# Kernel tuning notes

Measured on AMD Instinct MI355X. Metric: run time of the kernel, lower is better.

The kernel has to match this reference:

```python
import jax, jax.numpy as jnp
import numpy as np

D_MODEL = 256

def setup_inputs() -> dict:
    key = jax.random.key(0)
    k_x, k_wqkv, k_bqkv, k_wp, k_bp = jax.random.split(key, 5)
    B, T, d = 4, 4096, D_MODEL
    bound_qkv = 1.0 / np.sqrt(d)
    return {
        "x": jax.random.normal(k_x, (B, T, d), dtype=jnp.float32),
        "W_qkv": jax.random.uniform(k_wqkv, (d, 3 * d), jnp.float32, -bound_qkv, bound_qkv),
        "b_qkv": jax.random.uniform(k_bqkv, (3 * d,), jnp.float32, -bound_qkv, bound_qkv),
        "W_proj": jax.random.uniform(k_wp, (d, d), jnp.float32, -bound_qkv, bound_qkv),
        "b_proj": jax.random.uniform(k_bp, (d,), jnp.float32, -bound_qkv, bound_qkv),
    }

def reference(x, W_qkv, b_qkv, W_proj, b_proj):
    B, T, d = x.shape
    qkv = x @ W_qkv + b_qkv                       # (B, T, 3d)
    q, k, v = jnp.split(qkv, 3, axis=-1)          # each (B, T, d)
    scale = 1.0 / np.sqrt(d).astype(np.float32)
    scores = jnp.einsum('btd,bsd->bts', q, k) * scale   # (B, T, T)
    causal = jnp.tril(jnp.ones((T, T), dtype=bool))     # allowed positions
    scores = jnp.where(causal, scores, -jnp.inf)
    weights = jax.nn.softmax(scores, axis=-1)           # (B, T, T)
    ctx = jnp.einsum('bts,bsd->btd', weights, v)        # (B, T, d)
    return ctx @ W_proj + b_proj
```

## Files before the change

### kernel.cpp

```cpp
#include <hip/hip_runtime.h>
#include <math.h>

#define TT 4096
#define BB 4
#define DM 256
#define NSEG_B 80

typedef __attribute__((ext_vector_type(8))) short short8;
typedef __attribute__((ext_vector_type(4))) short short4v;
typedef __attribute__((ext_vector_type(4))) float f32x4;

#define MFMA16(a, b, c) __builtin_amdgcn_mfma_f32_16x16x32_bf16(a, b, c, 0, 0, 0)

#define GL2LDS(gp, lp) __builtin_amdgcn_global_load_lds( \
    (const __attribute__((address_space(1))) unsigned int*)(gp), \
    (__attribute__((address_space(3))) unsigned int*)(lp), 16, 0, 0)

__device__ __forceinline__ short f2b(float f) {
    union { float f; unsigned u; } v; v.f = f;
    unsigned r = v.u + 0x7FFFu + ((v.u >> 16) & 1u);
    return (short)(r >> 16);
}
__device__ __forceinline__ float b2f(short h) {
    union { unsigned u; float f; } v;
    v.u = ((unsigned)(unsigned short)h) << 16;
    return v.f;
}

__global__ __launch_bounds__(256) void transpose_cast2(
    const float* __restrict__ W1, short* __restrict__ Wt1,
    const float* __restrict__ W2, short* __restrict__ Wt2)
{
    __shared__ float T[64 * 68];
    const int tid = threadIdx.x;
    const int by = blockIdx.y;
    const float* W; short* Wt; int N, n0;
    if (by < 12) { W = W1; Wt = Wt1; N = 768; n0 = by * 64; }
    else         { W = W2; Wt = Wt2; N = 256; n0 = (by - 12) * 64; }
    const int k0 = blockIdx.x * 64;
#pragma unroll
    for (int it = 0; it < 4; ++it) {
        int idx = tid + it * 256;
        int r = idx >> 4, c4 = idx & 15;
        *(float4*)&T[r * 68 + c4 * 4] =
            *(const float4*)&W[(size_t)(k0 + r) * N + n0 + c4 * 4];
    }
    __syncthreads();
#pragma unroll
    for (int it = 0; it < 4; ++it) {
        int idx = tid + it * 256;
        int n = idx >> 4, c4 = idx & 15;
        short4v t;
#pragma unroll
        for (int j = 0; j < 4; ++j) t[j] = f2b(T[(c4 * 4 + j) * 68 + n]);
        *(short4v*)&Wt[(size_t)(n0 + n) * 256 + k0 + c4 * 4] = t;
    }
}

__global__ __launch_bounds__(256) void qkv_gemm(
    const float* __restrict__ x, const short* __restrict__ Bt,
    const float* __restrict__ bias, short* __restrict__ qkvb,
    short* __restrict__ VtG)
{
    __shared__ short As[16384];
    __shared__ short Bs[16384];
    __shared__ short Ts[64 * 72];

    const int tid = threadIdx.x;
    const int w = tid >> 6, lane = tid & 63;
    const int l15 = lane & 15, quad = lane >> 4;
    const int m0 = blockIdx.x * 64;
    const int nsup = blockIdx.y * 384;

#pragma unroll
    for (int it = 0; it < 8; ++it) {
        int idx = tid + it * 256;
        int row = ((idx >> 9) << 4) + (idx & 15);
        int col = ((idx >> 6) & 7) * 32 + ((idx >> 4) & 3) * 8;
        const float* src = &x[(size_t)(m0 + row) * 256 + col];
        float4 u = *(const float4*)src, u2 = *(const float4*)(src + 4);
        short8 t;
        t[0] = f2b(u.x);  t[1] = f2b(u.y);  t[2] = f2b(u.z);  t[3] = f2b(u.w);
        t[4] = f2b(u2.x); t[5] = f2b(u2.y); t[6] = f2b(u2.z); t[7] = f2b(u2.w);
        *(short8*)&As[idx * 8] = t;
    }

    for (int t6 = 0; t6 < 6; ++t6) {
        const int n0 = nsup + t6 * 64;
#pragma unroll
        for (int it = 0; it < 8; ++it) {
            int idx = tid + it * 256;
            int n = ((idx >> 9) << 4) + (idx & 15);
            int col = ((idx >> 6) & 7) * 32 + ((idx >> 4) & 3) * 8;
            *(short8*)&Bs[idx * 8] = *(const short8*)&Bt[(size_t)(n0 + n) * 256 + col];
        }
        __syncthreads();

        f32x4 acc[4];
#pragma unroll
        for (int t = 0; t < 4; ++t) acc[t] = (f32x4){0.f, 0.f, 0.f, 0.f};
#pragma unroll
        for (int k0 = 0; k0 < 8; ++k0) {
            short8 a = *(const short8*)&As[((w * 8 + k0) * 64 + lane) * 8];
#pragma unroll
            for (int nt = 0; nt < 4; ++nt) {
                short8 bb = *(const short8*)&Bs[((nt * 8 + k0) * 64 + lane) * 8];
                acc[nt] = MFMA16(a, bb, acc[nt]);
            }
        }

        if (n0 < 512) {
#pragma unroll
            for (int nt = 0; nt < 4; ++nt) {
                int n = n0 + nt * 16 + l15;
                float bv = bias[n];
#pragma unroll
                for (int r = 0; r < 4; ++r)
                    qkvb[(size_t)(m0 + w * 16 + quad * 4 + r) * 768 + n]
                        = f2b(acc[nt][r] + bv);
            }
            __syncthreads();
        } else {
#pragma unroll
            for (int nt = 0; nt < 4; ++nt) {
                int n = n0 + nt * 16 + l15;
                float bv = bias[n];
#pragma unroll
                for (int r = 0; r < 4; ++r)
                    Ts[(nt * 16 + l15) * 72 + w * 16 + quad * 4 + r]
                        = f2b(acc[nt][r] + bv);
            }
            __syncthreads();
            const int d  = tid >> 2;
            const int c  = tid & 3;
            short8 v0 = *(const short8*)&Ts[d * 72 + c * 16];
            short8 v1 = *(const short8*)&Ts[d * 72 + c * 16 + 8];
            const int bg = m0 >> 12, key0 = (m0 & 4095) + c * 16;
            short* dst = &VtG[((size_t)bg * 256 + (n0 - 512) + d) * 4096 + key0];
            *(short8*)dst = v0;
            *(short8*)(dst + 8) = v1;
        }
    }
}

__global__ __launch_bounds__(256, 2) void flash_mfma(
    const short* __restrict__ qkv,
    const short* __restrict__ VtG,
    short* __restrict__ Opart,
    float* __restrict__ L)
{
    __shared__ short Ks[2][4096];
    __shared__ short Vs[8192];
    __shared__ short Ps[4096];

    const int tid = threadIdx.x;
    const int w = tid >> 6, lane = tid & 63;
    const int l15 = lane & 15, quad = lane >> 4;

    const int b = blockIdx.x & 3;
    const int e = (NSEG_B - 1) - (blockIdx.x >> 2);
    const int lid = b * NSEG_B + e;
    int g = 0;
    while (g < 3 && e >= 4 * (g + 1) * (g + 2)) ++g;
    int off = e - 4 * g * (g + 1);
    int qt = 8 * g + off / (g + 1);
    int s  = off - (off / (g + 1)) * (g + 1);
    const int kp_lo = s * 32;
    const int kp_hi = min(kp_lo + 32, 4 * (qt + 1));
    const int npairs = kp_hi - kp_lo;

    const size_t base = (size_t)b * TT * 768;
    const int row0 = qt * 128;

    short8 aq[2][8];
#pragma unroll
    for (int rs = 0; rs < 2; ++rs) {
        const short* qrow = &qkv[base + (size_t)(row0 + rs * 64 + w * 16 + l15) * 768 + quad * 8];
#pragma unroll
        for (int k0 = 0; k0 < 8; ++k0)
            aq[rs][k0] = *(const short8*)&qrow[k0 * 32];
    }

#pragma unroll
    for (int it = 0; it < 2; ++it) {
        int idx = tid + it * 256;
        int row = idx & 15;
        int col = ((idx >> 6) & 7) * 32 + ((idx >> 4) & 3) * 8;
        GL2LDS(&qkv[base + (size_t)(kp_lo * 32 + row) * 768 + 256 + col], &Ks[0][idx * 8]);
    }

    f32x4 o[2][16];
#pragma unroll
    for (int rs = 0; rs < 2; ++rs)
#pragma unroll
        for (int c = 0; c < 16; ++c) o[rs][c] = (f32x4){0.f, 0.f, 0.f, 0.f};
    float l_acc[2][4] = {{0.f, 0.f, 0.f, 0.f}, {0.f, 0.f, 0.f, 0.f}};

    for (int u = 0; u < npairs; ++u) {
        const int j0 = (kp_lo + u) * 32;

        __syncthreads();

#pragma unroll
        for (int it = 0; it < 2; ++it) {
            int idx = tid + it * 256;
            int row = idx & 15;
            int col = ((idx >> 6) & 7) * 32 + ((idx >> 4) & 3) * 8;
            GL2LDS(&qkv[base + (size_t)(j0 + 16 + row) * 768 + 256 + col], &Ks[1][idx * 8]);
        }
        __builtin_amdgcn_sched_barrier(0);
#pragma unroll
        for (int it = 0; it < 4; ++it) {
            int idx = tid + it * 256;
            int d  = ((idx >> 6) << 4) + (idx & 15);
            int kc = ((idx >> 4) & 3) * 8;
            GL2LDS(&VtG[((size_t)b * 256 + d) * 4096 + j0 + kc], &Vs[idx * 8]);
        }
        __builtin_amdgcn_sched_barrier(0);

        {
            f32x4 s4[2];
            s4[0] = (f32x4){0.f, 0.f, 0.f, 0.f};
            s4[1] = (f32x4){0.f, 0.f, 0.f, 0.f};
#pragma unroll
            for (int k0 = 0; k0 < 8; ++k0) {
                short8 bb = *(const short8*)&Ks[0][(k0 * 64 + lane) * 8];
                s4[0] = MFMA16(aq[0][k0], bb, s4[0]);
                s4[1] = MFMA16(aq[1][k0], bb, s4[1]);
            }
#pragma unroll
            for (int rs = 0; rs < 2; ++rs)
#pragma unroll
                for (int r = 0; r < 4; ++r) {
                    const int rg = row0 + rs * 64 + w * 16 + quad * 4 + r;
                    int jg = j0 + l15;
                    float xx = s4[rs][r] * 0.0625f;
                    if (jg > rg) xx = -INFINITY;
                    float pv = __expf(fminf(xx, 30.f));
                    l_acc[rs][r] += pv;
                    Ps[((rs * 4 + w) * 64 + (0 * 2 + (l15 >> 3)) * 16 + quad * 4 + r) * 8
                       + (l15 & 7)] = f2b(pv);
                }
        }

        asm volatile("s_waitcnt vmcnt(4)" ::: "memory");
        __builtin_amdgcn_s_barrier();
        __builtin_amdgcn_sched_barrier(0);

        if (u + 1 < npairs) {
#pragma unroll
            for (int it = 0; it < 2; ++it) {
                int idx = tid + it * 256;
                int row = idx & 15;
                int col = ((idx >> 6) & 7) * 32 + ((idx >> 4) & 3) * 8;
                GL2LDS(&qkv[base + (size_t)(j0 + 32 + row) * 768 + 256 + col], &Ks[0][idx * 8]);
            }
        }
        __builtin_amdgcn_sched_barrier(0);

        {
            f32x4 s4[2];
            s4[0] = (f32x4){0.f, 0.f, 0.f, 0.f};
            s4[1] = (f32x4){0.f, 0.f, 0.f, 0.f};
#pragma unroll
            for (int k0 = 0; k0 < 8; ++k0) {
                short8 bb = *(const short8*)&Ks[1][(k0 * 64 + lane) * 8];
                s4[0] = MFMA16(aq[0][k0], bb, s4[0]);
                s4[1] = MFMA16(aq[1][k0], bb, s4[1]);
            }
#pragma unroll
            for (int rs = 0; rs < 2; ++rs)
#pragma unroll
                for (int r = 0; r < 4; ++r) {
                    const int rg = row0 + rs * 64 + w * 16 + quad * 4 + r;
                    int jg = j0 + 16 + l15;
                    float xx = s4[rs][r] * 0.0625f;
                    if (jg > rg) xx = -INFINITY;
                    float pv = __expf(fminf(xx, 30.f));
                    l_acc[rs][r] += pv;
                    Ps[((rs * 4 + w) * 64 + (1 * 2 + (l15 >> 3)) * 16 + quad * 4 + r) * 8
                       + (l15 & 7)] = f2b(pv);
                }
        }

        if (u + 1 < npairs) {
            asm volatile("s_waitcnt vmcnt(2)" ::: "memory");
        } else {
            asm volatile("s_waitcnt vmcnt(0)" ::: "memory");
        }
        __builtin_amdgcn_s_barrier();
        __builtin_amdgcn_sched_barrier(0);

        {
            short8 a0 = *(const short8*)&Ps[((0 * 4 + w) * 64 + lane) * 8];
            short8 a1 = *(const short8*)&Ps[((1 * 4 + w) * 64 + lane) * 8];
#pragma unroll
            for (int ct = 0; ct < 16; ++ct) {
                short8 bb = *(const short8*)&Vs[(ct * 64 + lane) * 8];
                o[0][ct] = MFMA16(a0, bb, o[0][ct]);
                o[1][ct] = MFMA16(a1, bb, o[1][ct]);
            }
        }
    }

#pragma unroll
    for (int rs = 0; rs < 2; ++rs)
#pragma unroll
        for (int r = 0; r < 4; ++r) {
            float l = l_acc[rs][r];
            l += __shfl_xor(l, 1); l += __shfl_xor(l, 2);
            l += __shfl_xor(l, 4); l += __shfl_xor(l, 8);
            if (l15 == 0)
                L[(size_t)lid * 128 + rs * 64 + w * 16 + quad * 4 + r] = l;
        }
    const size_t ob = (size_t)lid * (128 * 256);
#pragma unroll
    for (int rs = 0; rs < 2; ++rs)
#pragma unroll
        for (int r = 0; r < 4; ++r) {
            int lr = rs * 64 + w * 16 + quad * 4 + r;
#pragma unroll
            for (int c = 0; c < 16; ++c)
                Opart[ob + (size_t)lr * 256 + c * 16 + l15] = f2b(o[rs][c][r]);
        }
}

__global__ __launch_bounds__(256) void proj_gemm(
    const short* __restrict__ Opart, const float* __restrict__ L,
    const short* __restrict__ Bt, const float* __restrict__ bias,
    float* __restrict__ out)
{
    __shared__ short As[8192];
    __shared__ short Bs[16384];
    __shared__ float Linv[32];

    const int tid = threadIdx.x;
    const int w = tid >> 6, lane = tid & 63;
    const int l15 = lane & 15, quad = lane >> 4;
    const int t = blockIdx.x;
    const int b = t >> 7, q32 = t & 127;
    const int qt = q32 >> 2;
    const int ro = (q32 & 3) * 32;
    const int gg = qt >> 3, rr = qt & 7;
    const int sbase = b * NSEG_B + 4 * gg * (gg + 1) + rr * (gg + 1);
    const int nseg = gg + 1;
    const int m0 = t * 32;

    if (tid < 32) {
        float l = 0.f;
#pragma unroll
        for (int s2 = 0; s2 < 4; ++s2)
            if (s2 < nseg) l += L[(size_t)(sbase + s2) * 128 + ro + tid];
        Linv[tid] = 1.f / l;
    }
    __syncthreads();

#pragma unroll
    for (int it = 0; it < 4; ++it) {
        int idx = tid + it * 256;
        int row = ((idx >> 9) << 4) + (idx & 15);
        int col = ((idx >> 6) & 7) * 32 + ((idx >> 4) & 3) * 8;
        float a8[8] = {0.f, 0.f, 0.f, 0.f, 0.f, 0.f, 0.f, 0.f};
#pragma unroll
        for (int s2 = 0; s2 < 4; ++s2) {
            if (s2 < nseg) {
                short8 hv = *(const short8*)&Opart[(size_t)(sbase + s2) * 32768
                                                   + (size_t)(ro + row) * 256 + col];
#pragma unroll
                for (int j = 0; j < 8; ++j) a8[j] += b2f(hv[j]);
            }
        }
        float inv = Linv[row];
        short8 t8;
#pragma unroll
        for (int j = 0; j < 8; ++j) t8[j] = f2b(a8[j] * inv);
        *(short8*)&As[idx * 8] = t8;
    }

    for (int t2 = 0; t2 < 4; ++t2) {
        const int n0 = t2 * 64;
#pragma unroll
        for (int it = 0; it < 8; ++it) {
            int idx = tid + it * 256;
            int n = ((idx >> 9) << 4) + (idx & 15);
            int col = ((idx >> 6) & 7) * 32 + ((idx >> 4) & 3) * 8;
            *(short8*)&Bs[idx * 8] = *(const short8*)&Bt[(size_t)(n0 + n) * 256 + col];
        }
        __syncthreads();

        f32x4 acc[2];
        acc[0] = (f32x4){0.f, 0.f, 0.f, 0.f};
        acc[1] = (f32x4){0.f, 0.f, 0.f, 0.f};
#pragma unroll
        for (int k0 = 0; k0 < 8; ++k0) {
            short8 a = *(const short8*)&As[(((w & 1) * 8 + k0) * 64 + lane) * 8];
#pragma unroll
            for (int nt = 0; nt < 2; ++nt) {
                int n16 = (w >> 1) * 2 + nt;
                short8 bb = *(const short8*)&Bs[((n16 * 8 + k0) * 64 + lane) * 8];
                acc[nt] = MFMA16(a, bb, acc[nt]);
            }
        }
#pragma unroll
        for (int nt = 0; nt < 2; ++nt) {
            int n = n0 + ((w >> 1) * 2 + nt) * 16 + l15;
            float bv = bias[n];
#pragma unroll
            for (int r = 0; r < 4; ++r)
                out[(size_t)(m0 + (w & 1) * 16 + quad * 4 + r) * 256 + n] = acc[nt][r] + bv;
        }
        __syncthreads();
    }
}

extern "C" void kernel_launch(void* const* d_in, const int* in_sizes, int n_in,
                              void* d_out, int out_size, void* d_ws, size_t ws_size,
                              hipStream_t stream)
{
    const float* x     = (const float*)d_in[0];
    const float* Wqkv  = (const float*)d_in[1];
    const float* bqkv  = (const float*)d_in[2];
    const float* Wproj = (const float*)d_in[3];
    const float* bproj = (const float*)d_in[4];
    float* out = (float*)d_out;

    const size_t M = (size_t)BB * TT;
    short* qkv_b = (short*)d_ws;
    short* Wt1   = qkv_b + M * 768;
    short* Wt2   = Wt1 + (size_t)768 * 256;
    short* VtG   = Wt2 + (size_t)256 * 256;
    short* Opart = VtG + (size_t)BB * 256 * 4096;
    float* L     = (float*)(Opart + (size_t)BB * NSEG_B * 128 * 256);

    transpose_cast2<<<dim3(4, 16), dim3(256), 0, stream>>>(Wqkv, Wt1, Wproj, Wt2);
    qkv_gemm<<<dim3(256, 2), dim3(256), 0, stream>>>(x, Wt1, bqkv, qkv_b, VtG);
    flash_mfma<<<dim3(BB * NSEG_B), dim3(256), 0, stream>>>(qkv_b, VtG, Opart, L);
    proj_gemm<<<dim3(512), dim3(256), 0, stream>>>(Opart, L, Wt2, bproj, out);
}
```

Before: 211.5 us.

## Drop LDS staging and read K, V and weight operands directly from global

Removes the shared-memory staging buffers for the weight tiles in the QKV and projection GEMMs, and the double-buffered async global-to-LDS K/V pipeline in the attention kernel. MFMA B operands are now loaded straight from global memory (relying on cache), along with most block-wide barriers. The aim is to cut LDS footprint, copy and synchronisation overhead, and possibly raise occupancy. In exchange, each wave re-fetches K/V and weight data that was previously shared across the block, and the explicit prefetch overlap is lost.

Measured after the change: 387.0 us. 82.9% more time.

```diff
diff --git a/kernel.cpp b/kernel.cpp
--- a/kernel.cpp
+++ b/kernel.cpp
@@ -11,10 +11,6 @@
 typedef __attribute__((ext_vector_type(4))) float f32x4;
 
 #define MFMA16(a, b, c) __builtin_amdgcn_mfma_f32_16x16x32_bf16(a, b, c, 0, 0, 0)
-
-#define GL2LDS(gp, lp) __builtin_amdgcn_global_load_lds( \
-    (const __attribute__((address_space(1))) unsigned int*)(gp), \
-    (__attribute__((address_space(3))) unsigned int*)(lp), 16, 0, 0)
 
 __device__ __forceinline__ short f2b(float f) {
     union { float f; unsigned u; } v; v.f = f;
@@ -63,7 +59,6 @@
     short* __restrict__ VtG)
 {
     __shared__ short As[16384];
-    __shared__ short Bs[16384];
     __shared__ short Ts[64 * 72];
 
     const int tid = threadIdx.x;
@@ -84,17 +79,10 @@
         t[4] = f2b(u2.x); t[5] = f2b(u2.y); t[6] = f2b(u2.z); t[7] = f2b(u2.w);
         *(short8*)&As[idx * 8] = t;
     }
+    __syncthreads();
 
     for (int t6 = 0; t6 < 6; ++t6) {
         const int n0 = nsup + t6 * 64;
-#pragma unroll
-        for (int it = 0; it < 8; ++it) {
-            int idx = tid + it * 256;
-            int n = ((idx >> 9) << 4) + (idx & 15);
-            int col = ((idx >> 6) & 7) * 32 + ((idx >> 4) & 3) * 8;
-            *(short8*)&Bs[idx * 8] = *(const short8*)&Bt[(size_t)(n0 + n) * 256 + col];
-        }
-        __syncthreads();
 
         f32x4 acc[4];
 #pragma unroll
@@ -104,7 +92,8 @@
             short8 a = *(const short8*)&As[((w * 8 + k0) * 64 + lane) * 8];
 #pragma unroll
             for (int nt = 0; nt < 4; ++nt) {
-                short8 bb = *(const short8*)&Bs[((nt * 8 + k0) * 64 + lane) * 8];
+                short8 bb = *(const short8*)&Bt[(size_t)(n0 + nt * 16 + l15) * 256
+                                                + k0 * 32 + quad * 8];
                 acc[nt] = MFMA16(a, bb, acc[nt]);
             }
         }
@@ -119,8 +108,8 @@
                     qkvb[(size_t)(m0 + w * 16 + quad * 4 + r) * 768 + n]
                         = f2b(acc[nt][r] + bv);
             }
+        } else {
             __syncthreads();
-        } else {
 #pragma unroll
             for (int nt = 0; nt < 4; ++nt) {
                 int n = n0 + nt * 16 + l15;
@@ -149,8 +138,6 @@
     short* __restrict__ Opart,
     float* __restrict__ L)
 {
-    __shared__ short Ks[2][4096];
-    __shared__ short Vs[8192];
     __shared__ short Ps[4096];
 
     const int tid = threadIdx.x;
@@ -181,14 +168,6 @@
             aq[rs][k0] = *(const short8*)&qrow[k0 * 32];
     }
 
-#pragma unroll
-    for (int it = 0; it < 2; ++it) {
-        int idx = tid + it * 256;
-        int row = idx & 15;
-        int col = ((idx >> 6) & 7) * 32 + ((idx >> 4) & 3) * 8;
-        GL2LDS(&qkv[base + (size_t)(kp_lo * 32 + row) * 768 + 256 + col], &Ks[0][idx * 8]);
-    }
-
     f32x4 o[2][16];
 #pragma unroll
     for (int rs = 0; rs < 2; ++rs)
@@ -199,32 +178,15 @@
     for (int u = 0; u < npairs; ++u) {
         const int j0 = (kp_lo + u) * 32;
 
-        __syncthreads();
-
-#pragma unroll
-        for (int it = 0; it < 2; ++it) {
-            int idx = tid + it * 256;
-            int row = idx & 15;
-            int col = ((idx >> 6) & 7) * 32 + ((idx >> 4) & 3) * 8;
-            GL2LDS(&qkv[base + (size_t)(j0 + 16 + row) * 768 + 256 + col], &Ks[1][idx * 8]);
-        }
-        __builtin_amdgcn_sched_barrier(0);
-#pragma unroll
-        for (int it = 0; it < 4; ++it) {
-            int idx = tid + it * 256;
-            int d  = ((idx >> 6) << 4) + (idx & 15);
-            int kc = ((idx >> 4) & 3) * 8;
-            GL2LDS(&VtG[((size_t)b * 256 + d) * 4096 + j0 + kc], &Vs[idx * 8]);
-        }
-        __builtin_amdgcn_sched_barrier(0);
-
-        {
+#pragma unroll
+        for (int half = 0; half < 2; ++half) {
             f32x4 s4[2];
             s4[0] = (f32x4){0.f, 0.f, 0.f, 0.f};
             s4[1] = (f32x4){0.f, 0.f, 0.f, 0.f};
+            const short* krow = &qkv[base + (size_t)(j0 + half * 16 + l15) * 768 + 256 + quad * 8];
 #pragma unroll
             for (int k0 = 0; k0 < 8; ++k0) {
-                short8 bb = *(const short8*)&Ks[0][(k0 * 64 + lane) * 8];
+                short8 bb = *(const short8*)&krow[k0 * 32];
                 s4[0] = MFMA16(aq[0][k0], bb, s4[0]);
                 s4[1] = MFMA16(aq[1][k0], bb, s4[1]);
             }
@@ -233,70 +195,23 @@
 #pragma unroll
                 for (int r = 0; r < 4; ++r) {
                     const int rg = row0 + rs * 64 + w * 16 + quad * 4 + r;
-                    int jg = j0 + l15;
+                    int jg = j0 + half * 16 + l15;
                     float xx = s4[rs][r] * 0.0625f;
                     if (jg > rg) xx = -INFINITY;
                     float pv = __expf(fminf(xx, 30.f));
                     l_acc[rs][r] += pv;
-                    Ps[((rs * 4 + w) * 64 + (0 * 2 + (l15 >> 3)) * 16 + quad * 4 + r) * 8
+                    Ps[((rs * 4 + w) * 64 + (half * 2 + (l15 >> 3)) * 16 + quad * 4 + r) * 8
                        + (l15 & 7)] = f2b(pv);
                 }
         }
-
-        asm volatile("s_waitcnt vmcnt(4)" ::: "memory");
-        __builtin_amdgcn_s_barrier();
-        __builtin_amdgcn_sched_barrier(0);
-
-        if (u + 1 < npairs) {
-#pragma unroll
-            for (int it = 0; it < 2; ++it) {
-                int idx = tid + it * 256;
-                int row = idx & 15;
-                int col = ((idx >> 6) & 7) * 32 + ((idx >> 4) & 3) * 8;
-                GL2LDS(&qkv[base + (size_t)(j0 + 32 + row) * 768 + 256 + col], &Ks[0][idx * 8]);
-            }
-        }
-        __builtin_amdgcn_sched_barrier(0);
-
-        {
-            f32x4 s4[2];
-            s4[0] = (f32x4){0.f, 0.f, 0.f, 0.f};
-            s4[1] = (f32x4){0.f, 0.f, 0.f, 0.f};
-#pragma unroll
-            for (int k0 = 0; k0 < 8; ++k0) {
-                short8 bb = *(const short8*)&Ks[1][(k0 * 64 + lane) * 8];
-                s4[0] = MFMA16(aq[0][k0], bb, s4[0]);
-                s4[1] = MFMA16(aq[1][k0], bb, s4[1]);
-            }
-#pragma unroll
-            for (int rs = 0; rs < 2; ++rs)
-#pragma unroll
-                for (int r = 0; r < 4; ++r) {
-                    const int rg = row0 + rs * 64 + w * 16 + quad * 4 + r;
-                    int jg = j0 + 16 + l15;
-                    float xx = s4[rs][r] * 0.0625f;
-                    if (jg > rg) xx = -INFINITY;
-                    float pv = __expf(fminf(xx, 30.f));
-                    l_acc[rs][r] += pv;
-                    Ps[((rs * 4 + w) * 64 + (1 * 2 + (l15 >> 3)) * 16 + quad * 4 + r) * 8
-                       + (l15 & 7)] = f2b(pv);
-                }
-        }
-
-        if (u + 1 < npairs) {
-            asm volatile("s_waitcnt vmcnt(2)" ::: "memory");
-        } else {
-            asm volatile("s_waitcnt vmcnt(0)" ::: "memory");
-        }
-        __builtin_amdgcn_s_barrier();
-        __builtin_amdgcn_sched_barrier(0);
 
         {
             short8 a0 = *(const short8*)&Ps[((0 * 4 + w) * 64 + lane) * 8];
             short8 a1 = *(const short8*)&Ps[((1 * 4 + w) * 64 + lane) * 8];
 #pragma unroll
             for (int ct = 0; ct < 16; ++ct) {
-                short8 bb = *(const short8*)&Vs[(ct * 64 + lane) * 8];
+                short8 bb = *(const short8*)&VtG[((size_t)b * 256 + ct * 16 + l15) * 4096
+                                                 + j0 + quad * 8];
                 o[0][ct] = MFMA16(a0, bb, o[0][ct]);
                 o[1][ct] = MFMA16(a1, bb, o[1][ct]);
             }
@@ -331,7 +246,6 @@
     float* __restrict__ out)
 {
     __shared__ short As[8192];
-    __shared__ short Bs[16384];
     __shared__ float Linv[32];
 
     const int tid = threadIdx.x;
@@ -376,18 +290,10 @@
         for (int j = 0; j < 8; ++j) t8[j] = f2b(a8[j] * inv);
         *(short8*)&As[idx * 8] = t8;
     }
+    __syncthreads();
 
     for (int t2 = 0; t2 < 4; ++t2) {
         const int n0 = t2 * 64;
-#pragma unroll
-        for (int it = 0; it < 8; ++it) {
-            int idx = tid + it * 256;
-            int n = ((idx >> 9) << 4) + (idx & 15);
-            int col = ((idx >> 6) & 7) * 32 + ((idx >> 4) & 3) * 8;
-            *(short8*)&Bs[idx * 8] = *(const short8*)&Bt[(size_t)(n0 + n) * 256 + col];
-        }
-        __syncthreads();
-
         f32x4 acc[2];
         acc[0] = (f32x4){0.f, 0.f, 0.f, 0.f};
         acc[1] = (f32x4){0.f, 0.f, 0.f, 0.f};
@@ -397,7 +303,8 @@
 #pragma unroll
             for (int nt = 0; nt < 2; ++nt) {
                 int n16 = (w >> 1) * 2 + nt;
-                short8 bb = *(const short8*)&Bs[((n16 * 8 + k0) * 64 + lane) * 8];
+                short8 bb = *(const short8*)&Bt[(size_t)(n0 + n16 * 16 + l15) * 256
+                                                + k0 * 32 + quad * 8];
                 acc[nt] = MFMA16(a, bb, acc[nt]);
             }
         }
@@ -409,7 +316,6 @@
             for (int r = 0; r < 4; ++r)
                 out[(size_t)(m0 + (w & 1) * 16 + quad * 4 + r) * 256 + n] = acc[nt][r] + bv;
         }
-        __syncthreads();
     }
 }
 
```
